# Kernel optimization log

Measured on AMD Instinct MI355X. Metric: run time of the kernel, lower is better.

## Reference

```python
import jax, jax.numpy as jnp
import numpy as np

BS, L, NPH, NQ, H = 64, 512, 16, 16, 1024
EPS = 1e-5

def _ln(x, g, b):
    m = jnp.mean(x, axis=-1, keepdims=True)
    v = jnp.mean((x - m) ** 2, axis=-1, keepdims=True)
    return (x - m) * jax.lax.rsqrt(v + EPS) * g + b

def setup_inputs() -> dict:
    key = jax.random.key(0)
    ks = jax.random.split(key, 24)
    s = 0.02
    inp = {
        "lang_context_feat": jax.random.normal(ks[0], (BS, L, H), jnp.float32),
        "lang_query_feat": jax.random.normal(ks[1], (BS, NPH, H), jnp.float32),
        "mask_query_context": jax.random.randint(ks[2], (BS, NPH, L), 0, 2).astype(bool),
        "query_embed": jax.random.normal(ks[3], (NQ, 2 * H), jnp.float32) * s,
        # linear1/2/3: hidden -> hidden (stored [in, out])
        "W1": jax.random.normal(ks[4], (H, H), jnp.float32) * s, "b1": jnp.zeros((H,), jnp.float32),
        "W2": jax.random.normal(ks[5], (H, H), jnp.float32) * s, "b2": jnp.zeros((H,), jnp.float32),
        "W3": jax.random.normal(ks[6], (H, H), jnp.float32) * s, "b3": jnp.zeros((H,), jnp.float32),
        # context_out: Linear(h,h) + LayerNorm(h)
        "Wc": jax.random.normal(ks[7], (H, H), jnp.float32) * s, "bc": jnp.zeros((H,), jnp.float32),
        "gc": jnp.ones((H,), jnp.float32), "betac": jnp.zeros((H,), jnp.float32),
        # fuse_encoder_query: Linear(2h,h)+LN+ReLU+Dropout(eval)+Linear(h,h)+LN+ReLU
        "Wf1": jax.random.normal(ks[8], (2 * H, H), jnp.float32) * s, "bf1": jnp.zeros((H,), jnp.float32),
        "gf1": jnp.ones((H,), jnp.float32), "betaf1": jnp.zeros((H,), jnp.float32),
        "Wf2": jax.random.normal(ks[9], (H, H), jnp.float32) * s, "bf2": jnp.zeros((H,), jnp.float32),
        "gf2": jnp.ones((H,), jnp.float32), "betaf2": jnp.zeros((H,), jnp.float32),
    }
    return inp

def reference(lang_context_feat, lang_query_feat, mask_query_context,
              query_embed, W1, b1, W2, b2, W3, b3,
              Wc, bc, gc, betac,
              Wf1, bf1, gf1, betaf1, Wf2, bf2, gf2, betaf2):
    # single-query attention: k from first context token, q/v from all tokens
    k = lang_context_feat[:, 0:1, :] @ W1 + b1          # [bs,1,h]
    q = lang_context_feat @ W2 + b2                     # [bs,L,h]
    v = lang_context_feat @ W3 + b3                     # [bs,L,h]
    att = jnp.einsum("bih,blh->bil", k, q)             # [bs,1,L]
    att = jnp.broadcast_to(att, mask_query_context.shape)  # [bs,n_ph,L]
    att = jnp.where(mask_query_context, -jnp.inf, att)
    p = jax.nn.softmax(att, axis=-1)                    # [bs,n_ph,L]
    ctx = jnp.einsum("bpl,blh->bph", p, v)             # [bs,n_ph,h]
    ctx = _ln(ctx @ Wc + bc, gc, betac)
    ctx = lang_context_feat[:, None, 0, :] + ctx        # residual with first token
    x = jnp.concatenate([ctx, lang_query_feat], axis=-1)   # [bs,n_ph,2h]
    x = jax.nn.relu(_ln(x @ Wf1 + bf1, gf1, betaf1))        # dropout: eval mode (identity)
    x = jax.nn.relu(_ln(x @ Wf2 + bf2, gf2, betaf2))        # [bs,n_ph,h]
    # repeat(1,1,1,2) on last dim == tile [x, x]
    pq = jnp.concatenate([x, x], axis=-1)[:, :, None, :]    # [bs,n_ph,1,2h]
    pq = pq + query_embed[None, None, :, :]                 # [bs,n_ph,n_q,2h]
    pq = pq.reshape(pq.shape[0], -1, 2 * H).transpose(1, 0, 2)  # [n_ph*n_q,bs,2h]
    return pq[..., :H], pq[..., H:]
```

## Files before the change

### kernel.cpp

```cpp
#include <hip/hip_runtime.h>

typedef __bf16 bf16;
typedef __bf16 bf16x8 __attribute__((ext_vector_type(8)));
typedef __bf16 bf16x4 __attribute__((ext_vector_type(4)));
typedef float f32x4 __attribute__((ext_vector_type(4)));

#define BSZ 64
#define LCTX 512
#define NPH 16
#define NQ 16
#define HD 1024

__global__ __launch_bounds__(256) void tconv_kernel(const float* __restrict__ W,
                                                    bf16* __restrict__ Wt, int K, int N) {
    __shared__ float tile[32][33];
    int k0 = blockIdx.x * 32, n0 = blockIdx.y * 32;
    int t = threadIdx.x, c = t & 31, r = t >> 5;
#pragma unroll
    for (int i = 0; i < 4; i++) {
        int kr = r + i * 8;
        tile[kr][c] = W[(size_t)(k0 + kr) * N + n0 + c];
    }
    __syncthreads();
#pragma unroll
    for (int i = 0; i < 4; i++) {
        int nr = r + i * 8;
        Wt[(size_t)(n0 + nr) * K + k0 + c] = (bf16)tile[c][nr];
    }
}

__global__ __launch_bounds__(256) void lqconv_kernel(const float* __restrict__ lq,
                                                     bf16* __restrict__ X) {
    int i = blockIdx.x * 256 + threadIdx.x;
    if (i >= 262144) return;
    float4 v = ((const float4*)lq)[i];
    int row = i >> 8, h4 = i & 255;
    bf16x4 o = {(bf16)v.x, (bf16)v.y, (bf16)v.z, (bf16)v.w};
    *(bf16x4*)(X + (size_t)row * 2048 + 1024 + h4 * 4) = o;
}

__global__ void detect_kernel(const unsigned int* __restrict__ mask, int* __restrict__ flag) {
    if (threadIdx.x == 0) {
        int s = 4;
        for (int i = 0; i < 128; i++)
            if (mask[i] > 1u) { s = 1; break; }
        *flag = s;
    }
}

__global__ __launch_bounds__(256) void kpart_kernel(const float* __restrict__ x,
                                                    const float* __restrict__ W1,
                                                    float* __restrict__ partial) {
    __shared__ float xs[64][68];
    __shared__ float ws[64][64];
    int n0 = blockIdx.x * 64, k0 = blockIdx.y * 64;
    int t = threadIdx.x;
#pragma unroll
    for (int i = 0; i < 4; i++) {
        int f = t + i * 256;
        int b = f >> 4, c = f & 15;
        *(float4*)&xs[b][c * 4] =
            *(const float4*)(x + (size_t)b * LCTX * HD + k0 + c * 4);
    }
#pragma unroll
    for (int i = 0; i < 4; i++) {
        int f = t + i * 256;
        int r = f >> 4, c = f & 15;
        *(float4*)&ws[r][c * 4] =
            *(const float4*)(W1 + (size_t)(k0 + r) * 1024 + n0 + c * 4);
    }
    __syncthreads();
    int tb = t >> 4, tc = t & 15;
    int b0 = tb * 4;
    float acc[4][4] = {};
    for (int kk = 0; kk < 64; kk += 4) {
        float4 w0 = *(const float4*)&ws[kk + 0][tc * 4];
        float4 w1 = *(const float4*)&ws[kk + 1][tc * 4];
        float4 w2 = *(const float4*)&ws[kk + 2][tc * 4];
        float4 w3 = *(const float4*)&ws[kk + 3][tc * 4];
        float4 xv[4];
#pragma unroll
        for (int bi = 0; bi < 4; bi++) xv[bi] = *(const float4*)&xs[b0 + bi][kk];
#pragma unroll
        for (int bi = 0; bi < 4; bi++) {
            acc[bi][0] += xv[bi].x * w0.x + xv[bi].y * w1.x + xv[bi].z * w2.x + xv[bi].w * w3.x;
            acc[bi][1] += xv[bi].x * w0.y + xv[bi].y * w1.y + xv[bi].z * w2.y + xv[bi].w * w3.y;
            acc[bi][2] += xv[bi].x * w0.z + xv[bi].y * w1.z + xv[bi].z * w2.z + xv[bi].w * w3.z;
            acc[bi][3] += xv[bi].x * w0.w + xv[bi].y * w1.w + xv[bi].z * w2.w + xv[bi].w * w3.w;
        }
    }
    float* pout = partial + ((size_t)blockIdx.y * 64 + b0) * 1024 + n0 + tc * 4;
#pragma unroll
    for (int bi = 0; bi < 4; bi++) {
        float4 o = make_float4(acc[bi][0], acc[bi][1], acc[bi][2], acc[bi][3]);
        *(float4*)(pout + (size_t)bi * 1024) = o;
    }
}

__global__ __launch_bounds__(256) void kreduce_kernel(const float* __restrict__ partial,
                                                      const float* __restrict__ b1,
                                                      float* __restrict__ kout) {
    int b = blockIdx.x, t = threadIdx.x;
    float4 acc = ((const float4*)b1)[t];
#pragma unroll
    for (int kt = 0; kt < 16; kt++) {
        float4 v = ((const float4*)(partial + ((size_t)kt * 64 + b) * 1024))[t];
        acc.x += v.x; acc.y += v.y; acc.z += v.z; acc.w += v.w;
    }
    ((float4*)(kout + (size_t)b * 1024))[t] = acc;
}

__global__ __launch_bounds__(256) void mmat_kernel(const float* __restrict__ kin,
                                                   const float* __restrict__ W2,
                                                   float* __restrict__ mout) {
    __shared__ float ks[1024];
    int b = blockIdx.x, i0 = blockIdx.y * 64, t = threadIdx.x;
    *(float4*)&ks[t * 4] = ((const float4*)(kin + (size_t)b * 1024))[t];
    __syncthreads();
    int wave = t >> 6, lane = t & 63;
    for (int rr = 0; rr < 16; rr++) {
        int i = i0 + wave * 16 + rr;
        const float* wrow = W2 + (size_t)i * 1024;
        float s = 0.f;
#pragma unroll
        for (int j = 0; j < 4; j++) {
            float4 wv = ((const float4*)wrow)[lane + j * 64];
            const float4 kv = *(const float4*)&ks[(lane + j * 64) * 4];
            s += wv.x * kv.x + wv.y * kv.y + wv.z * kv.z + wv.w * kv.w;
        }
        for (int off = 32; off; off >>= 1) s += __shfl_xor(s, off, 64);
        if (lane == 0) mout[(size_t)b * 1024 + i] = s;
    }
}

__global__ __launch_bounds__(256) void att_kernel(const float* __restrict__ x,
                                                  const float* __restrict__ m,
                                                  float* __restrict__ att) {
    __shared__ float ms[1024];
    int b = blockIdx.x, l0 = blockIdx.y * 64, t = threadIdx.x;
    *(float4*)&ms[t * 4] = ((const float4*)(m + (size_t)b * 1024))[t];
    __syncthreads();
    int wave = t >> 6, lane = t & 63;
    for (int rr = 0; rr < 16; rr++) {
        int l = l0 + wave * 16 + rr;
        const float* xr = x + ((size_t)b * LCTX + l) * HD;
        float s = 0.f;
#pragma unroll
        for (int j = 0; j < 4; j++) {
            float4 xv = ((const float4*)xr)[lane + j * 64];
            const float4 mv = *(const float4*)&ms[(lane + j * 64) * 4];
            s += xv.x * mv.x + xv.y * mv.y + xv.z * mv.z + xv.w * mv.w;
        }
        for (int off = 32; off; off >>= 1) s += __shfl_xor(s, off, 64);
        if (lane == 0) att[(size_t)b * LCTX + l] = s;
    }
}

__global__ __launch_bounds__(256) void softmax_kernel(const float* __restrict__ att,
                                                      const unsigned char* __restrict__ mask,
                                                      const int* __restrict__ flagp,
                                                      float* __restrict__ p) {
    __shared__ float red1[8], red2[8];
    int bp = blockIdx.x, b = bp >> 4, t = threadIdx.x;
    int stride = flagp[0];
    size_t base = (size_t)bp * LCTX;
    bool mk0 = mask[(base + t) * (size_t)stride] != 0;
    bool mk1 = mask[(base + t + 256) * (size_t)stride] != 0;
    float a0 = mk0 ? -1e30f : att[(size_t)b * LCTX + t];
    float a1 = mk1 ? -1e30f : att[(size_t)b * LCTX + t + 256];
    float mx = fmaxf(a0, a1);
    for (int off = 32; off; off >>= 1) mx = fmaxf(mx, __shfl_xor(mx, off, 64));
    int wave = t >> 6, lane = t & 63;
    if (lane == 0) red1[wave] = mx;
    __syncthreads();
    mx = fmaxf(fmaxf(red1[0], red1[1]), fmaxf(red1[2], red1[3]));
    float e0 = mk0 ? 0.f : expf(a0 - mx);
    float e1 = mk1 ? 0.f : expf(a1 - mx);
    float s = e0 + e1;
    for (int off = 32; off; off >>= 1) s += __shfl_xor(s, off, 64);
    if (lane == 0) red2[wave] = s;
    __syncthreads();
    s = red2[0] + red2[1] + red2[2] + red2[3];
    float inv = 1.f / s;
    p[base + t] = e0 * inv;
    p[base + t + 256] = e1 * inv;
}

__global__ __launch_bounds__(256) void y_kernel(const float* __restrict__ x,
                                                const float* __restrict__ p,
                                                bf16* __restrict__ y) {
    __shared__ float ps[16][512];
    int b = blockIdx.x, c0 = blockIdx.y * 256, t = threadIdx.x;
    const float4* pp = (const float4*)(p + (size_t)b * 16 * 512);
    float4* psv = (float4*)ps;
    for (int i = t; i < 2048; i += 256) psv[i] = pp[i];
    __syncthreads();
    float acc[16] = {};
    const float* xb = x + (size_t)b * LCTX * HD + c0 + t;
    for (int l = 0; l < 512; l++) {
        float xv = xb[(size_t)l * HD];
#pragma unroll
        for (int q = 0; q < 16; q++) acc[q] += ps[q][l] * xv;
    }
#pragma unroll
    for (int q = 0; q < 16; q++)
        y[((size_t)(b * 16 + q)) * HD + c0 + t] = (bf16)acc[q];
}

template <bool OUT_BF16>
__global__ __launch_bounds__(256) void gemm_kernel(const bf16* __restrict__ A, int lda,
                                                   const bf16* __restrict__ Bt, int ldb,
                                                   const float* __restrict__ bias,
                                                   void* __restrict__ Cv, int ldc,
                                                   int M, int N, int K) {
    __shared__ bf16 sA[64][40];
    __shared__ bf16 sB[64][40];
    int tid = threadIdx.x;
    int wave = tid >> 6, lane = tid & 63;
    int m0 = blockIdx.x * 64, n0 = blockIdx.y * 64;
    int wr = (wave >> 1) * 32, wc = (wave & 1) * 32;
    int lrow = tid >> 2, lk = (tid & 3) * 8;
    int l16 = lane & 15, lhi = lane >> 4;
    f32x4 acc[2][2] = {};
    for (int k0 = 0; k0 < K; k0 += 32) {
        bf16x8 av = *(const bf16x8*)(A + (size_t)(m0 + lrow) * lda + k0 + lk);
        bf16x8 bv = *(const bf16x8*)(Bt + (size_t)(n0 + lrow) * ldb + k0 + lk);
        __syncthreads();
        *(bf16x8*)&sA[lrow][lk] = av;
        *(bf16x8*)&sB[lrow][lk] = bv;
        __syncthreads();
        bf16x8 a0 = *(const bf16x8*)&sA[wr + l16][lhi * 8];
        bf16x8 a1 = *(const bf16x8*)&sA[wr + 16 + l16][lhi * 8];
        bf16x8 b0 = *(const bf16x8*)&sB[wc + l16][lhi * 8];
        bf16x8 b1 = *(const bf16x8*)&sB[wc + 16 + l16][lhi * 8];
        acc[0][0] = __builtin_amdgcn_mfma_f32_16x16x32_bf16(a0, b0, acc[0][0], 0, 0, 0);
        acc[0][1] = __builtin_amdgcn_mfma_f32_16x16x32_bf16(a0, b1, acc[0][1], 0, 0, 0);
        acc[1][0] = __builtin_amdgcn_mfma_f32_16x16x32_bf16(a1, b0, acc[1][0], 0, 0, 0);
        acc[1][1] = __builtin_amdgcn_mfma_f32_16x16x32_bf16(a1, b1, acc[1][1], 0, 0, 0);
    }
#pragma unroll
    for (int mi = 0; mi < 2; mi++)
#pragma unroll
        for (int ni = 0; ni < 2; ni++)
#pragma unroll
            for (int r = 0; r < 4; r++) {
                int row = m0 + wr + mi * 16 + lhi * 4 + r;
                int col = n0 + wc + ni * 16 + l16;
                float v = acc[mi][ni][r] + bias[col];
                if (OUT_BF16)
                    ((bf16*)Cv)[(size_t)row * ldc + col] = (bf16)v;
                else
                    ((float*)Cv)[(size_t)row * ldc + col] = v;
            }
}

template <int MODE>
__global__ __launch_bounds__(256) void ln_kernel(const float* __restrict__ C,
                                                 const float* __restrict__ g,
                                                 const float* __restrict__ beta,
                                                 const float* __restrict__ resid,
                                                 void* __restrict__ out) {
    __shared__ float r1[8], r2[8];
    int row = blockIdx.x, t = threadIdx.x;
    float4 v = ((const float4*)(C + (size_t)row * 1024))[t];
    float s = v.x + v.y + v.z + v.w;
    float s2 = v.x * v.x + v.y * v.y + v.z * v.z + v.w * v.w;
    for (int off = 32; off; off >>= 1) {
        s += __shfl_xor(s, off, 64);
        s2 += __shfl_xor(s2, off, 64);
    }
    int wave = t >> 6, lane = t & 63;
    if (lane == 0) { r1[wave] = s; r2[wave] = s2; }
    __syncthreads();
    float S = r1[0] + r1[1] + r1[2] + r1[3];
    float S2 = r2[0] + r2[1] + r2[2] + r2[3];
    float mean = S * (1.f / 1024.f);
    float var = S2 * (1.f / 1024.f) - mean * mean;
    float inv = rsqrtf(var + 1e-5f);
    float4 gv = ((const float4*)g)[t];
    float4 bv = ((const float4*)beta)[t];
    float o[4];
    o[0] = (v.x - mean) * inv * gv.x + bv.x;
    o[1] = (v.y - mean) * inv * gv.y + bv.y;
    o[2] = (v.z - mean) * inv * gv.z + bv.z;
    o[3] = (v.w - mean) * inv * gv.w + bv.w;
    if (MODE == 0) {
        int b = row >> 4;
        const float* x0 = resid + (size_t)b * LCTX * HD + t * 4;
        bf16x4 w = {(bf16)(o[0] + x0[0]), (bf16)(o[1] + x0[1]),
                    (bf16)(o[2] + x0[2]), (bf16)(o[3] + x0[3])};
        *(bf16x4*)((bf16*)out + (size_t)row * 2048 + t * 4) = w;
    } else if (MODE == 1) {
        bf16x4 w = {(bf16)fmaxf(o[0], 0.f), (bf16)fmaxf(o[1], 0.f),
                    (bf16)fmaxf(o[2], 0.f), (bf16)fmaxf(o[3], 0.f)};
        *(bf16x4*)((bf16*)out + (size_t)row * 1024 + t * 4) = w;
    } else {
        float4 w = make_float4(fmaxf(o[0], 0.f), fmaxf(o[1], 0.f),
                               fmaxf(o[2], 0.f), fmaxf(o[3], 0.f));
        ((float4*)((float*)out + (size_t)row * 1024))[t] = w;
    }
}

__global__ __launch_bounds__(256) void out_kernel(const float* __restrict__ t2,
                                                  const float* __restrict__ qe,
                                                  float* __restrict__ out) {
    const size_t total4 = 8388608;
    const size_t half4 = 4194304;
    for (size_t i = (size_t)blockIdx.x * 256 + threadIdx.x; i < total4;
         i += (size_t)gridDim.x * 256) {
        int half = i >= half4;
        size_t r = half ? i - half4 : i;
        int h4 = (int)(r & 255);
        size_t rb = r >> 8;
        int b = (int)(rb & 63);
        int pq = (int)(rb >> 6);
        int pp = pq >> 4, q = pq & 15;
        float4 tv = ((const float4*)(t2 + ((size_t)(b * 16 + pp)) * 1024))[h4];
        float4 qv = ((const float4*)(qe + (size_t)q * 2048 + (half ? 1024 : 0)))[h4];
        float4 o = make_float4(tv.x + qv.x, tv.y + qv.y, tv.z + qv.z, tv.w + qv.w);
        ((float4*)out)[i] = o;
    }
}

extern "C" void kernel_launch(void* const* d_in, const int* in_sizes, int n_in,
                              void* d_out, int out_size, void* d_ws, size_t ws_size,
                              hipStream_t stream) {
    const float* x      = (const float*)d_in[0];
    const float* lq     = (const float*)d_in[1];
    const unsigned char* mask = (const unsigned char*)d_in[2];
    const float* qe     = (const float*)d_in[3];
    const float* W1     = (const float*)d_in[4];
    const float* b1     = (const float*)d_in[5];
    const float* W2     = (const float*)d_in[6];
    const float* W3     = (const float*)d_in[8];
    const float* b3     = (const float*)d_in[9];
    const float* Wc     = (const float*)d_in[10];
    const float* bc     = (const float*)d_in[11];
    const float* gc     = (const float*)d_in[12];
    const float* betac  = (const float*)d_in[13];
    const float* Wf1    = (const float*)d_in[14];
    const float* bf1    = (const float*)d_in[15];
    const float* gf1    = (const float*)d_in[16];
    const float* betaf1 = (const float*)d_in[17];
    const float* Wf2    = (const float*)d_in[18];
    const float* bf2    = (const float*)d_in[19];
    const float* gf2    = (const float*)d_in[20];
    const float* betaf2 = (const float*)d_in[21];

    char* ws = (char*)d_ws;
    const size_t MB = 1 << 20;
    bf16* W3t   = (bf16*)(ws + 0 * MB);
    bf16* Wct   = (bf16*)(ws + 2 * MB);
    bf16* Wf1t  = (bf16*)(ws + 4 * MB);
    bf16* Wf2t  = (bf16*)(ws + 8 * MB);
    bf16* X     = (bf16*)(ws + 10 * MB);
    float* kbuf = (float*)(ws + 14 * MB);
    float* mbuf = (float*)(ws + 14 * MB + 256 * 1024);
    float* attb = (float*)(ws + 14 * MB + 512 * 1024);
    int* flag   = (int*)(ws + 14 * MB + 768 * 1024);
    float* pbuf = (float*)(ws + 15 * MB);
    bf16* ybuf  = (bf16*)(ws + 17 * MB);
    bf16* ctxp  = (bf16*)(ws + 19 * MB);
    float* Cbuf = (float*)(ws + 21 * MB);
    bf16* t1    = (bf16*)(ws + 25 * MB);
    float* t2   = (float*)(ws + 27 * MB);
    float* kpartial = Cbuf;

    tconv_kernel<<<dim3(32, 32), 256, 0, stream>>>(W3, W3t, 1024, 1024);
    tconv_kernel<<<dim3(32, 32), 256, 0, stream>>>(Wc, Wct, 1024, 1024);
    tconv_kernel<<<dim3(64, 32), 256, 0, stream>>>(Wf1, Wf1t, 2048, 1024);
    tconv_kernel<<<dim3(32, 32), 256, 0, stream>>>(Wf2, Wf2t, 1024, 1024);
    lqconv_kernel<<<1024, 256, 0, stream>>>(lq, X);
    detect_kernel<<<1, 64, 0, stream>>>((const unsigned int*)mask, flag);
    kpart_kernel<<<dim3(16, 16), 256, 0, stream>>>(x, W1, kpartial);
    kreduce_kernel<<<64, 256, 0, stream>>>(kpartial, b1, kbuf);
    mmat_kernel<<<dim3(64, 16), 256, 0, stream>>>(kbuf, W2, mbuf);
    att_kernel<<<dim3(64, 8), 256, 0, stream>>>(x, mbuf, attb);
    softmax_kernel<<<1024, 256, 0, stream>>>(attb, mask, flag, pbuf);
    y_kernel<<<dim3(64, 4), 256, 0, stream>>>(x, pbuf, ybuf);
    gemm_kernel<true><<<dim3(16, 16), 256, 0, stream>>>(ybuf, 1024, W3t, 1024, b3,
                                                        ctxp, 1024, 1024, 1024, 1024);
    gemm_kernel<false><<<dim3(16, 16), 256, 0, stream>>>(ctxp, 1024, Wct, 1024, bc,
                                                         Cbuf, 1024, 1024, 1024, 1024);
    ln_kernel<0><<<1024, 256, 0, stream>>>(Cbuf, gc, betac, x, X);
    gemm_kernel<false><<<dim3(16, 16), 256, 0, stream>>>(X, 2048, Wf1t, 2048, bf1,
                                                         Cbuf, 1024, 1024, 1024, 2048);
    ln_kernel<1><<<1024, 256, 0, stream>>>(Cbuf, gf1, betaf1, nullptr, t1);
    gemm_kernel<false><<<dim3(16, 16), 256, 0, stream>>>(t1, 1024, Wf2t, 1024, bf2,
                                                         Cbuf, 1024, 1024, 1024, 1024);
    ln_kernel<2><<<1024, 256, 0, stream>>>(Cbuf, gf2, betaf2, nullptr, t2);
    out_kernel<<<2048, 256, 0, stream>>>(t2, qe, (float*)d_out);
}
```

Before: 256.6 us.

## Fuse prep kernels, pipeline GEMM with async LDS loads, fuse final LN with output

After: 231.0 us. 10.0% less time.

```diff
diff --git a/kernel.cpp b/kernel.cpp
--- a/kernel.cpp
+++ b/kernel.cpp
@@ -11,40 +11,37 @@
 #define NQ 16
 #define HD 1024
 
-__global__ __launch_bounds__(256) void tconv_kernel(const float* __restrict__ W,
-                                                    bf16* __restrict__ Wt, int K, int N) {
+__global__ __launch_bounds__(256) void prep_kernel(const float* __restrict__ W3,
+                                                   const float* __restrict__ Wc,
+                                                   const float* __restrict__ Wf1,
+                                                   const float* __restrict__ Wf2,
+                                                   const float* __restrict__ lq,
+                                                   bf16* __restrict__ W3t, bf16* __restrict__ Wct,
+                                                   bf16* __restrict__ Wf1t, bf16* __restrict__ Wf2t,
+                                                   bf16* __restrict__ X) {
     __shared__ float tile[32][33];
-    int k0 = blockIdx.x * 32, n0 = blockIdx.y * 32;
-    int t = threadIdx.x, c = t & 31, r = t >> 5;
-#pragma unroll
-    for (int i = 0; i < 4; i++) {
-        int kr = r + i * 8;
-        tile[kr][c] = W[(size_t)(k0 + kr) * N + n0 + c];
-    }
-    __syncthreads();
-#pragma unroll
-    for (int i = 0; i < 4; i++) {
-        int nr = r + i * 8;
-        Wt[(size_t)(n0 + nr) * K + k0 + c] = (bf16)tile[c][nr];
-    }
-}
-
-__global__ __launch_bounds__(256) void lqconv_kernel(const float* __restrict__ lq,
-                                                     bf16* __restrict__ X) {
-    int i = blockIdx.x * 256 + threadIdx.x;
-    if (i >= 262144) return;
-    float4 v = ((const float4*)lq)[i];
-    int row = i >> 8, h4 = i & 255;
-    bf16x4 o = {(bf16)v.x, (bf16)v.y, (bf16)v.z, (bf16)v.w};
-    *(bf16x4*)(X + (size_t)row * 2048 + 1024 + h4 * 4) = o;
-}
-
-__global__ void detect_kernel(const unsigned int* __restrict__ mask, int* __restrict__ flag) {
-    if (threadIdx.x == 0) {
-        int s = 4;
-        for (int i = 0; i < 128; i++)
-            if (mask[i] > 1u) { s = 1; break; }
-        *flag = s;
+    int blk = blockIdx.x, t = threadIdx.x;
+    if (blk < 5120) {
+        const float* W; bf16* Wt; int K, N, i;
+        if (blk < 1024)      { W = W3;  Wt = W3t;  K = 1024; N = 1024; i = blk; }
+        else if (blk < 2048) { W = Wc;  Wt = Wct;  K = 1024; N = 1024; i = blk - 1024; }
+        else if (blk < 3072) { W = Wf2; Wt = Wf2t; K = 1024; N = 1024; i = blk - 2048; }
+        else                 { W = Wf1; Wt = Wf1t; K = 2048; N = 1024; i = blk - 3072; }
+        int k0 = (i >> 5) * 32, n0 = (i & 31) * 32;
+        int c = t & 31, r = t >> 5;
+#pragma unroll
+        for (int j = 0; j < 4; j++)
+            tile[r + j * 8][c] = W[(size_t)(k0 + r + j * 8) * N + n0 + c];
+        __syncthreads();
+#pragma unroll
+        for (int j = 0; j < 4; j++)
+            Wt[(size_t)(n0 + r + j * 8) * K + k0 + c] = (bf16)tile[c][r + j * 8];
+    } else {
+        int i = (blk - 5120) * 256 + t;
+        float4 v = ((const float4*)lq)[i];
+        int row = i >> 8, h4 = i & 255;
+        bf16x4 o = {(bf16)v.x, (bf16)v.y, (bf16)v.z, (bf16)v.w};
+        *(bf16x4*)(X + (size_t)row * 2048 + 1024 + h4 * 4) = o;
     }
 }
 
@@ -158,11 +155,15 @@
 
 __global__ __launch_bounds__(256) void softmax_kernel(const float* __restrict__ att,
                                                       const unsigned char* __restrict__ mask,
-                                                      const int* __restrict__ flagp,
                                                       float* __restrict__ p) {
     __shared__ float red1[8], red2[8];
+    __shared__ int sstr;
     int bp = blockIdx.x, b = bp >> 4, t = threadIdx.x;
-    int stride = flagp[0];
+    if (t == 0) sstr = 4;
+    __syncthreads();
+    if (t < 128 && ((const unsigned int*)mask)[t] > 1u) sstr = 1;
+    __syncthreads();
+    int stride = sstr;
     size_t base = (size_t)bp * LCTX;
     bool mk0 = mask[(base + t) * (size_t)stride] != 0;
     bool mk1 = mask[(base + t + 256) * (size_t)stride] != 0;
@@ -207,37 +208,71 @@
         y[((size_t)(b * 16 + q)) * HD + c0 + t] = (bf16)acc[q];
 }
 
+__device__ __forceinline__ void gl16(const bf16* g, bf16* l) {
+    __builtin_amdgcn_global_load_lds((const __attribute__((address_space(1))) void*)g,
+                                     (__attribute__((address_space(3))) void*)l, 16, 0, 0);
+}
+__device__ __forceinline__ bf16x8 ldsfrag(const bf16* base, int row, int kb) {
+    return *(const bf16x8*)(base + row * 64 + ((kb ^ (row & 7)) << 3));
+}
+
 template <bool OUT_BF16>
 __global__ __launch_bounds__(256) void gemm_kernel(const bf16* __restrict__ A, int lda,
                                                    const bf16* __restrict__ Bt, int ldb,
                                                    const float* __restrict__ bias,
-                                                   void* __restrict__ Cv, int ldc,
-                                                   int M, int N, int K) {
-    __shared__ bf16 sA[64][40];
-    __shared__ bf16 sB[64][40];
+                                                   void* __restrict__ Cv, int ldc, int K) {
+    __shared__ bf16 sA[2][4096];
+    __shared__ bf16 sB[2][4096];
     int tid = threadIdx.x;
     int wave = tid >> 6, lane = tid & 63;
     int m0 = blockIdx.x * 64, n0 = blockIdx.y * 64;
     int wr = (wave >> 1) * 32, wc = (wave & 1) * 32;
-    int lrow = tid >> 2, lk = (tid & 3) * 8;
     int l16 = lane & 15, lhi = lane >> 4;
-    f32x4 acc[2][2] = {};
-    for (int k0 = 0; k0 < K; k0 += 32) {
-        bf16x8 av = *(const bf16x8*)(A + (size_t)(m0 + lrow) * lda + k0 + lk);
-        bf16x8 bv = *(const bf16x8*)(Bt + (size_t)(n0 + lrow) * ldb + k0 + lk);
+
+    int r0 = tid >> 3, kb = tid & 7;
+    int r1 = r0 + 32;
+    int sk0 = (kb ^ (r0 & 7)) << 3;
+    int sk1 = (kb ^ (r1 & 7)) << 3;
+    const bf16* A0 = A + (size_t)(m0 + r0) * lda + sk0;
+    const bf16* A1 = A + (size_t)(m0 + r1) * lda + sk1;
+    const bf16* B0 = Bt + (size_t)(n0 + r0) * ldb + sk0;
+    const bf16* B1 = Bt + (size_t)(n0 + r1) * ldb + sk1;
+    int wb0 = (wave * 64) * 8;
+    int wb1 = (256 + wave * 64) * 8;
+
+    f32x4 acc00 = {}, acc01 = {}, acc10 = {}, acc11 = {};
+
+    int nt = K >> 6;
+    gl16(A0, &sA[0][wb0]); gl16(A1, &sA[0][wb1]);
+    gl16(B0, &sB[0][wb0]); gl16(B1, &sB[0][wb1]);
+    asm volatile("s_waitcnt vmcnt(0)" ::: "memory");
+    __syncthreads();
+    int cur = 0;
+    for (int tI = 0; tI < nt; ++tI) {
+        if (tI + 1 < nt) {
+            int ko = (tI + 1) << 6;
+            gl16(A0 + ko, &sA[cur ^ 1][wb0]); gl16(A1 + ko, &sA[cur ^ 1][wb1]);
+            gl16(B0 + ko, &sB[cur ^ 1][wb0]); gl16(B1 + ko, &sB[cur ^ 1][wb1]);
+        }
+        const bf16* a = sA[cur];
+        const bf16* bt = sB[cur];
+#pragma unroll
+        for (int ks = 0; ks < 2; ks++) {
+            int kbb = ks * 4 + lhi;
+            bf16x8 a0 = ldsfrag(a, wr + l16, kbb);
+            bf16x8 a1v = ldsfrag(a, wr + 16 + l16, kbb);
+            bf16x8 b0v = ldsfrag(bt, wc + l16, kbb);
+            bf16x8 b1v = ldsfrag(bt, wc + 16 + l16, kbb);
+            acc00 = __builtin_amdgcn_mfma_f32_16x16x32_bf16(a0, b0v, acc00, 0, 0, 0);
+            acc01 = __builtin_amdgcn_mfma_f32_16x16x32_bf16(a0, b1v, acc01, 0, 0, 0);
+            acc10 = __builtin_amdgcn_mfma_f32_16x16x32_bf16(a1v, b0v, acc10, 0, 0, 0);
+            acc11 = __builtin_amdgcn_mfma_f32_16x16x32_bf16(a1v, b1v, acc11, 0, 0, 0);
+        }
+        asm volatile("s_waitcnt vmcnt(0)" ::: "memory");
         __syncthreads();
-        *(bf16x8*)&sA[lrow][lk] = av;
-        *(bf16x8*)&sB[lrow][lk] = bv;
-        __syncthreads();
-        bf16x8 a0 = *(const bf16x8*)&sA[wr + l16][lhi * 8];
-        bf16x8 a1 = *(const bf16x8*)&sA[wr + 16 + l16][lhi * 8];
-        bf16x8 b0 = *(const bf16x8*)&sB[wc + l16][lhi * 8];
-        bf16x8 b1 = *(const bf16x8*)&sB[wc + 16 + l16][lhi * 8];
-        acc[0][0] = __builtin_amdgcn_mfma_f32_16x16x32_bf16(a0, b0, acc[0][0], 0, 0, 0);
-        acc[0][1] = __builtin_amdgcn_mfma_f32_16x16x32_bf16(a0, b1, acc[0][1], 0, 0, 0);
-        acc[1][0] = __builtin_amdgcn_mfma_f32_16x16x32_bf16(a1, b0, acc[1][0], 0, 0, 0);
-        acc[1][1] = __builtin_amdgcn_mfma_f32_16x16x32_bf16(a1, b1, acc[1][1], 0, 0, 0);
-    }
+        cur ^= 1;
+    }
+    f32x4 accs[2][2] = {{acc00, acc01}, {acc10, acc11}};
 #pragma unroll
     for (int mi = 0; mi < 2; mi++)
 #pragma unroll
@@ -246,7 +281,7 @@
             for (int r = 0; r < 4; r++) {
                 int row = m0 + wr + mi * 16 + lhi * 4 + r;
                 int col = n0 + wc + ni * 16 + l16;
-                float v = acc[mi][ni][r] + bias[col];
+                float v = accs[mi][ni][r] + bias[col];
                 if (OUT_BF16)
                     ((bf16*)Cv)[(size_t)row * ldc + col] = (bf16)v;
                 else
@@ -290,35 +325,54 @@
         bf16x4 w = {(bf16)(o[0] + x0[0]), (bf16)(o[1] + x0[1]),
                     (bf16)(o[2] + x0[2]), (bf16)(o[3] + x0[3])};
         *(bf16x4*)((bf16*)out + (size_t)row * 2048 + t * 4) = w;
-    } else if (MODE == 1) {
+    } else {
         bf16x4 w = {(bf16)fmaxf(o[0], 0.f), (bf16)fmaxf(o[1], 0.f),
                     (bf16)fmaxf(o[2], 0.f), (bf16)fmaxf(o[3], 0.f)};
         *(bf16x4*)((bf16*)out + (size_t)row * 1024 + t * 4) = w;
-    } else {
-        float4 w = make_float4(fmaxf(o[0], 0.f), fmaxf(o[1], 0.f),
-                               fmaxf(o[2], 0.f), fmaxf(o[3], 0.f));
-        ((float4*)((float*)out + (size_t)row * 1024))[t] = w;
-    }
-}
-
-__global__ __launch_bounds__(256) void out_kernel(const float* __restrict__ t2,
-                                                  const float* __restrict__ qe,
-                                                  float* __restrict__ out) {
-    const size_t total4 = 8388608;
-    const size_t half4 = 4194304;
-    for (size_t i = (size_t)blockIdx.x * 256 + threadIdx.x; i < total4;
-         i += (size_t)gridDim.x * 256) {
-        int half = i >= half4;
-        size_t r = half ? i - half4 : i;
-        int h4 = (int)(r & 255);
-        size_t rb = r >> 8;
-        int b = (int)(rb & 63);
-        int pq = (int)(rb >> 6);
-        int pp = pq >> 4, q = pq & 15;
-        float4 tv = ((const float4*)(t2 + ((size_t)(b * 16 + pp)) * 1024))[h4];
-        float4 qv = ((const float4*)(qe + (size_t)q * 2048 + (half ? 1024 : 0)))[h4];
-        float4 o = make_float4(tv.x + qv.x, tv.y + qv.y, tv.z + qv.z, tv.w + qv.w);
-        ((float4*)out)[i] = o;
+    }
+}
+
+__global__ __launch_bounds__(256) void lnout_kernel(const float* __restrict__ C,
+                                                    const float* __restrict__ g,
+                                                    const float* __restrict__ beta,
+                                                    const float* __restrict__ qe,
+                                                    float* __restrict__ out) {
+    __shared__ float r1[8], r2[8];
+    int row = blockIdx.x, t = threadIdx.x;
+    int b = row >> 4, pp = row & 15;
+    float4 v = ((const float4*)(C + (size_t)row * 1024))[t];
+    float s = v.x + v.y + v.z + v.w;
+    float s2 = v.x * v.x + v.y * v.y + v.z * v.z + v.w * v.w;
+    for (int off = 32; off; off >>= 1) {
+        s += __shfl_xor(s, off, 64);
+        s2 += __shfl_xor(s2, off, 64);
+    }
+    int wave = t >> 6, lane = t & 63;
+    if (lane == 0) { r1[wave] = s; r2[wave] = s2; }
+    __syncthreads();
+    float S = r1[0] + r1[1] + r1[2] + r1[3];
+    float S2 = r2[0] + r2[1] + r2[2] + r2[3];
+    float mean = S * (1.f / 1024.f);
+    float var = S2 * (1.f / 1024.f) - mean * mean;
+    float inv = rsqrtf(var + 1e-5f);
+    float4 gv = ((const float4*)g)[t];
+    float4 bv = ((const float4*)beta)[t];
+    float4 ov;
+    ov.x = fmaxf((v.x - mean) * inv * gv.x + bv.x, 0.f);
+    ov.y = fmaxf((v.y - mean) * inv * gv.y + bv.y, 0.f);
+    ov.z = fmaxf((v.z - mean) * inv * gv.z + bv.z, 0.f);
+    ov.w = fmaxf((v.w - mean) * inv * gv.w + bv.w, 0.f);
+    float* out0 = out;
+    float* out1 = out + (size_t)256 * 64 * 1024;
+#pragma unroll
+    for (int q = 0; q < 16; q++) {
+        float4 q0 = ((const float4*)(qe + (size_t)q * 2048))[t];
+        float4 q1 = ((const float4*)(qe + (size_t)q * 2048 + 1024))[t];
+        size_t orow = ((size_t)(pp * 16 + q) * 64 + b) * 1024;
+        float4 w0 = make_float4(ov.x + q0.x, ov.y + q0.y, ov.z + q0.z, ov.w + q0.w);
+        float4 w1 = make_float4(ov.x + q1.x, ov.y + q1.y, ov.z + q1.z, ov.w + q1.w);
+        ((float4*)(out0 + orow))[t] = w0;
+        ((float4*)(out1 + orow))[t] = w1;
     }
 }
 
@@ -357,37 +411,29 @@
     float* kbuf = (float*)(ws + 14 * MB);
     float* mbuf = (float*)(ws + 14 * MB + 256 * 1024);
     float* attb = (float*)(ws + 14 * MB + 512 * 1024);
-    int* flag   = (int*)(ws + 14 * MB + 768 * 1024);
     float* pbuf = (float*)(ws + 15 * MB);
     bf16* ybuf  = (bf16*)(ws + 17 * MB);
     bf16* ctxp  = (bf16*)(ws + 19 * MB);
     float* Cbuf = (float*)(ws + 21 * MB);
     bf16* t1    = (bf16*)(ws + 25 * MB);
-    float* t2   = (float*)(ws + 27 * MB);
     float* kpartial = Cbuf;
 
-    tconv_kernel<<<dim3(32, 32), 256, 0, stream>>>(W3, W3t, 1024, 1024);
-    tconv_kernel<<<dim3(32, 32), 256, 0, stream>>>(Wc, Wct, 1024, 1024);
-    tconv_kernel<<<dim3(64, 32), 256, 0, stream>>>(Wf1, Wf1t, 2048, 1024);
-    tconv_kernel<<<dim3(32, 32), 256, 0, stream>>>(Wf2, Wf2t, 1024, 1024);
-    lqconv_kernel<<<1024, 256, 0, stream>>>(lq, X);
-    detect_kernel<<<1, 64, 0, stream>>>((const unsigned int*)mask, flag);
+    prep_kernel<<<6144, 256, 0, stream>>>(W3, Wc, Wf1, Wf2, lq, W3t, Wct, Wf1t, Wf2t, X);
     kpart_kernel<<<dim3(16, 16), 256, 0, stream>>>(x, W1, kpartial);
     kreduce_kernel<<<64, 256, 0, stream>>>(kpartial, b1, kbuf);
     mmat_kernel<<<dim3(64, 16), 256, 0, stream>>>(kbuf, W2, mbuf);
     att_kernel<<<dim3(64, 8), 256, 0, stream>>>(x, mbuf, attb);
-    softmax_kernel<<<1024, 256, 0, stream>>>(attb, mask, flag, pbuf);
+    softmax_kernel<<<1024, 256, 0, stream>>>(attb, mask, pbuf);
     y_kernel<<<dim3(64, 4), 256, 0, stream>>>(x, pbuf, ybuf);
     gemm_kernel<true><<<dim3(16, 16), 256, 0, stream>>>(ybuf, 1024, W3t, 1024, b3,
-                                                        ctxp, 1024, 1024, 1024, 1024);
+                                                        ctxp, 1024, 1024);
     gemm_kernel<false><<<dim3(16, 16), 256, 0, stream>>>(ctxp, 1024, Wct, 1024, bc,
-                                                         Cbuf, 1024, 1024, 1024, 1024);
+                                                         Cbuf, 1024, 1024);
     ln_kernel<0><<<1024, 256, 0, stream>>>(Cbuf, gc, betac, x, X);
     gemm_kernel<false><<<dim3(16, 16), 256, 0, stream>>>(X, 2048, Wf1t, 2048, bf1,
-                                                         Cbuf, 1024, 1024, 1024, 2048);
+                                                         Cbuf, 1024, 2048);
     ln_kernel<1><<<1024, 256, 0, stream>>>(Cbuf, gf1, betaf1, nullptr, t1);
     gemm_kernel<false><<<dim3(16, 16), 256, 0, stream>>>(t1, 1024, Wf2t, 1024, bf2,
-                                                         Cbuf, 1024, 1024, 1024, 1024);
-    ln_kernel<2><<<1024, 256, 0, stream>>>(Cbuf, gf2, betaf2, nullptr, t2);
-    out_kernel<<<2048, 256, 0, stream>>>(t2, qe, (float*)d_out);
-}
+                                                         Cbuf, 1024, 1024);
+    lnout_kernel<<<1024, 256, 0, stream>>>(Cbuf, gf2, betaf2, qe, (float*)d_out);
+}
```
